# Performance work log

Hardware: AMD Instinct MI355X
Metric: run time of the kernel (lower is better)

Reference implementation:

```python
import jax, jax.numpy as jnp
import numpy as np

BSZ, T, D_IN, P, H, D_OUT = 8, 4096, 512, 256, 256, 512


def setup_inputs() -> dict:
    key = jax.random.key(0)
    ks = jax.random.split(key, 8)
    x_seq = jax.random.normal(ks[0], (BSZ, T, D_IN), dtype=jnp.float32)
    # stable diagonal transition: |a| < 1 so the 4096-step recurrence does not blow up
    a = jax.random.uniform(ks[1], (H,), minval=-0.99, maxval=0.99, dtype=jnp.float32)
    B = jax.random.normal(ks[2], (P, H), dtype=jnp.float32) * 0.05
    C = jax.random.normal(ks[3], (H, P), dtype=jnp.float32) * 0.05
    Wi = jax.random.normal(ks[4], (P, D_IN), dtype=jnp.float32) * 0.05
    bi = jax.random.normal(ks[5], (P,), dtype=jnp.float32) * 0.05
    Wo = jax.random.normal(ks[6], (D_OUT, P), dtype=jnp.float32) * 0.05
    bo = jax.random.normal(ks[7], (D_OUT,), dtype=jnp.float32) * 0.05
    return {"x_seq": x_seq, "a": a, "B": B, "C": C, "Wi": Wi, "bi": bi, "Wo": Wo, "bo": bo}


def reference(x_seq, a, B, C, Wi, bi, Wo, bo):
    # proj_in + relu (eqx.nn.Linear: y = W @ x + b), vmapped over batch and time
    x_proj = jax.nn.relu(jnp.einsum("btd,pd->btp", x_seq, Wi) + bi)  # [Bsz,T,P]
    # precompute driving input u_t = B^T x_t for every step
    u = jnp.einsum("btp,ph->bth", x_proj, B)  # [Bsz,T,H]
    u_t = jnp.swapaxes(u, 0, 1)  # [T,Bsz,H] (scan over time)

    def step(h, u_step):  # h: [Bsz,H]
        h = a * h + u_step
        return h, h

    h0 = jnp.zeros((x_seq.shape[0], a.shape[0]), dtype=x_seq.dtype)
    _, hs = jax.lax.scan(step, h0, u_t)  # hs: [T,Bsz,H]
    # y_t = C^T h_t, then proj_out
    y_seq = jnp.einsum("tbh,hp->btp", hs, C)  # [Bsz,T,P]
    y_out = jnp.einsum("btp,op->bto", y_seq, Wo) + bo  # [Bsz,T,D_out]
    return y_out
```

## Files before the change

### kernel.cpp

```cpp
#include <hip/hip_runtime.h>

#define BSZN 8
#define TT 4096
#define DIN 512
#define PP 256
#define HHH 256
#define DOUT 512
#define LCH 64
#define NCH (TT / LCH)
#define NBLK (BSZN * NCH)
#define XPS 264
#define AST 136

typedef __attribute__((ext_vector_type(8))) short bf16x8;
typedef __attribute__((ext_vector_type(4))) float f32x4;

#define GLOBAL_AS __attribute__((address_space(1)))
#define LDS_AS __attribute__((address_space(3)))

static __device__ __forceinline__ void gld_lds16(const void* g, void* l) {
  __builtin_amdgcn_global_load_lds((const GLOBAL_AS unsigned int*)g,
                                   (LDS_AS unsigned int*)l, 16, 0, 0);
}

static __device__ __forceinline__ unsigned short f2bf(float x) {
  union { float f; unsigned u; } t{x};
  unsigned r = t.u + 0x7fffu + ((t.u >> 16) & 1u);
  return (unsigned short)(r >> 16);
}

static __device__ __forceinline__ float ld_carry(const float* p) {
  return __hip_atomic_load(p, __ATOMIC_RELAXED, __HIP_MEMORY_SCOPE_AGENT);
}


__global__ __launch_bounds__(256) void prep_k(
    const float* __restrict__ Wi, const float* __restrict__ Wo,
    const float* __restrict__ Cm, const float* __restrict__ Bm,
    unsigned short* __restrict__ Wi_t, unsigned short* __restrict__ B_t,
    unsigned short* __restrict__ C_t, unsigned short* __restrict__ Wo_t,
    int* __restrict__ flag_g) {
  const int b = blockIdx.x, tid = threadIdx.x;
  if (b < 128) {
    const int idx = b * 1024 + tid * 4;
    const int row = idx >> 9, d = idx & 511;
    const float4 v = *(const float4*)(Wi + idx);
    uint2 w;
    w.x = (unsigned)f2bf(v.x) | ((unsigned)f2bf(v.y) << 16);
    w.y = (unsigned)f2bf(v.z) | ((unsigned)f2bf(v.w) << 16);
    const int tile = d >> 5, kc = (d >> 3) & 3, s = (kc + (row >> 1)) & 3;
    *(uint2*)(Wi_t + tile * 8192 + row * 32 + s * 8 + (d & 7)) = w;
  } else if (b < 192) {
    const int f = (b - 128) * 256 + tid;
    const int p = f >> 6, h = (f & 63) * 4;
    const float4 v = *(const float4*)(Bm + (size_t)p * HHH + h);
    const float vv[4] = {v.x, v.y, v.z, v.w};
    const int tile = p >> 5, kc = (p >> 3) & 3;
#pragma unroll
    for (int j = 0; j < 4; ++j) {
      const int row = h + j, s = (kc + (row >> 1)) & 3;
      B_t[tile * 8192 + row * 32 + s * 8 + (p & 7)] = f2bf(vv[j]);
    }
  } else if (b < 256) {
    const int f = (b - 192) * 256 + tid;
    const int h = f >> 6, p = (f & 63) * 4;
    const float4 v = *(const float4*)(Cm + (size_t)h * PP + p);
    const float vv[4] = {v.x, v.y, v.z, v.w};
    const int tile = h >> 5, kc = (h >> 3) & 3;
#pragma unroll
    for (int j = 0; j < 4; ++j) {
      const int row = p + j, s = (kc + (row >> 1)) & 3;
      C_t[tile * 8192 + row * 32 + s * 8 + (h & 7)] = f2bf(vv[j]);
    }
  } else if (b < 384) {
    const int idx = (b - 256) * 1024 + tid * 4;
    const int o = idx >> 8, p = idx & 255;
    const float4 v = *(const float4*)(Wo + idx);
    uint2 w;
    w.x = (unsigned)f2bf(v.x) | ((unsigned)f2bf(v.y) << 16);
    w.y = (unsigned)f2bf(v.z) | ((unsigned)f2bf(v.w) << 16);
    const int tile = p >> 5, kc = (p >> 3) & 3, s = (kc + (o >> 1)) & 3;
    *(uint2*)(Wo_t + tile * 16384 + o * 32 + s * 8 + (p & 7)) = w;
  } else {
    flag_g[tid] = 0;
    flag_g[tid + 256] = 0;
  }
}

__global__ __launch_bounds__(256, 2) void s4_mega(
    const float* __restrict__ x, const float* __restrict__ a,
    const unsigned short* __restrict__ Wi_t, const float* __restrict__ bi,
    const unsigned short* __restrict__ B_t,
    const unsigned short* __restrict__ C_t,
    const unsigned short* __restrict__ Wo_t, const float* __restrict__ bo,
    float* __restrict__ out, float* __restrict__ carry_g,
    int* __restrict__ flag_g) {
  __shared__ alignas(16) char smem[67584];
  char* As = smem;
  unsigned short* xp = (unsigned short*)smem;
  char* TB = smem + 33792;
  float* PL = (float*)(smem + 66560);

  const int tid = threadIdx.x, wave = tid >> 6, lane = tid & 63;
  const int l15 = lane & 15, q = lane >> 4;
  const int bc = blockIdx.x, b = bc >> 6, c = bc & (NCH - 1);
  const size_t row0 = (size_t)bc * LCH;
  const int wc = wave * 64;

  int wrot[4];
#pragma unroll
  for (int ni = 0; ni < 4; ++ni) {
    const int r = wc + ni * 16 + l15;
    wrot[ni] = r * 64 + (((q + (r >> 1)) & 3) << 4);
  }
  int crot[2][4];
#pragma unroll
  for (int g = 0; g < 2; ++g)
#pragma unroll
    for (int ni = 0; ni < 4; ++ni) {
      const int r = wave * 128 + g * 64 + ni * 16 + l15;
      crot[g][ni] = r * 64 + (((q + (r >> 1)) & 3) << 4);
    }
  int afb[4];
#pragma unroll
  for (int mi = 0; mi < 4; ++mi) afb[mi] = (mi * 16 + l15) * AST + q * 16;
  int xpb[4];
#pragma unroll
  for (int mi = 0; mi < 4; ++mi) xpb[mi] = (mi * 16 + l15) * XPS + q * 8;

  const int sbase = wave * 4096 + lane * 16;

  f32x4 acc[4][4];
#pragma unroll
  for (int i = 0; i < 4; ++i)
#pragma unroll
    for (int j = 0; j < 4; ++j) acc[i][j] = f32x4{0.f, 0.f, 0.f, 0.f};

  float4 xv[4];
#pragma unroll
  for (int i = 0; i < 4; ++i) {
    const int f = i * 256 + tid;
    xv[i] = *(const float4*)(x + (row0 + (f >> 4)) * DIN + (f & 15) * 4);
  }
  for (int t = 0; t < 8; ++t) {
#pragma unroll
    for (int i = 0; i < 4; ++i) {
      const int f = i * 256 + tid;
      uint2 w;
      w.x = (unsigned)f2bf(xv[i].x) | ((unsigned)f2bf(xv[i].y) << 16);
      w.y = (unsigned)f2bf(xv[i].z) | ((unsigned)f2bf(xv[i].w) << 16);
      *(uint2*)(As + (f >> 4) * AST + (f & 15) * 8) = w;
    }
    {
      const char* gw = (const char*)Wi_t + t * 32768 + sbase;
#pragma unroll
      for (int i = 0; i < 4; ++i) {
        gld_lds16(gw + i * 1024, TB + sbase + i * 1024);
        gld_lds16(gw + 16384 + i * 1024, TB + 16384 + sbase + i * 1024);
      }
    }
    __syncthreads();
    if (t < 7) {
#pragma unroll
      for (int i = 0; i < 4; ++i) {
        const int f = i * 256 + tid;
        xv[i] = *(const float4*)(x + (row0 + (f >> 4)) * DIN + (t + 1) * 64 +
                                 (f & 15) * 4);
      }
    }
    bf16x8 af[4][2], bfv[4][2];
#pragma unroll
    for (int mi = 0; mi < 4; ++mi) {
      af[mi][0] = *(const bf16x8*)(As + afb[mi]);
      af[mi][1] = *(const bf16x8*)(As + afb[mi] + 64);
    }
#pragma unroll
    for (int ni = 0; ni < 4; ++ni) {
      bfv[ni][0] = *(const bf16x8*)(TB + wrot[ni]);
      bfv[ni][1] = *(const bf16x8*)(TB + 16384 + wrot[ni]);
    }
#pragma unroll
    for (int kk = 0; kk < 2; ++kk)
#pragma unroll
      for (int mi = 0; mi < 4; ++mi)
#pragma unroll
        for (int ni = 0; ni < 4; ++ni)
          acc[mi][ni] = __builtin_amdgcn_mfma_f32_16x16x32_bf16(
              af[mi][kk], bfv[ni][kk], acc[mi][ni], 0, 0, 0);
    __syncthreads();
  }

  {
    const char* gw = (const char*)B_t + sbase;
#pragma unroll
    for (int i = 0; i < 4; ++i) {
      gld_lds16(gw + i * 1024, TB + sbase + i * 1024);
      gld_lds16(gw + 16384 + i * 1024, TB + 16384 + sbase + i * 1024);
    }
  }

#pragma unroll
  for (int ni = 0; ni < 4; ++ni) {
    const int col = wc + ni * 16 + l15;
    const float bb = bi[col];
#pragma unroll
    for (int mi = 0; mi < 4; ++mi)
#pragma unroll
      for (int reg = 0; reg < 4; ++reg) {
        const int row = mi * 16 + q * 4 + reg;
        xp[row * XPS + col] = f2bf(fmaxf(acc[mi][ni][reg] + bb, 0.f));
      }
  }

#pragma unroll
  for (int i = 0; i < 4; ++i)
#pragma unroll
    for (int j = 0; j < 4; ++j) acc[i][j] = f32x4{0.f, 0.f, 0.f, 0.f};
  for (int t = 0; t < 4; ++t) {
    if (t > 0) {
      const char* gw = (const char*)B_t + t * 32768 + sbase;
#pragma unroll
      for (int i = 0; i < 4; ++i) {
        gld_lds16(gw + i * 1024, TB + sbase + i * 1024);
        gld_lds16(gw + 16384 + i * 1024, TB + 16384 + sbase + i * 1024);
      }
    }
    __syncthreads();
    bf16x8 af[4][2], bfv[4][2];
#pragma unroll
    for (int mi = 0; mi < 4; ++mi) {
      af[mi][0] = *(const bf16x8*)(xp + xpb[mi] + t * 64);
      af[mi][1] = *(const bf16x8*)(xp + xpb[mi] + t * 64 + 32);
    }
#pragma unroll
    for (int ni = 0; ni < 4; ++ni) {
      bfv[ni][0] = *(const bf16x8*)(TB + wrot[ni]);
      bfv[ni][1] = *(const bf16x8*)(TB + 16384 + wrot[ni]);
    }
#pragma unroll
    for (int kk = 0; kk < 2; ++kk)
#pragma unroll
      for (int mi = 0; mi < 4; ++mi)
#pragma unroll
        for (int ni = 0; ni < 4; ++ni)
          acc[mi][ni] = __builtin_amdgcn_mfma_f32_16x16x32_bf16(
              af[mi][kk], bfv[ni][kk], acc[mi][ni], 0, 0, 0);
    __syncthreads();
  }

  float aC[4], Wz[4];
#pragma unroll
  for (int ni = 0; ni < 4; ++ni) aC[ni] = a[wc + ni * 16 + l15];
#pragma unroll
  for (int ni = 0; ni < 4; ++ni) {
    const float A = aC[ni];
    const float A2 = A * A, A4 = A2 * A2, A8 = A4 * A4, A16 = A8 * A8;
    const float A4q = ((q & 1) ? A4 : 1.f) * ((q & 2) ? A8 : 1.f);
    float W = 0.f;
#pragma unroll
    for (int mi = 0; mi < 4; ++mi) {
      f32x4 v = acc[mi][ni];
      v.y = fmaf(A, v.x, v.y);
      v.z = fmaf(A, v.y, v.z);
      v.w = fmaf(A, v.z, v.w);
      const float E = v.w;
      const float E0 = __shfl(E, l15, 64);
      const float E1 = __shfl(E, l15 + 16, 64);
      const float E2 = __shfl(E, l15 + 32, 64);
      const float E3 = __shfl(E, l15 + 48, 64);
      const float s1 = E0, s2 = fmaf(A4, s1, E1), s3 = fmaf(A4, s2, E2);
      const float s4 = fmaf(A4, s3, E3);
      const float Sq = (q == 0) ? 0.f : (q == 1) ? s1 : (q == 2) ? s2 : s3;
      const float sin_ = fmaf(A4q, W, Sq);
      v.x = fmaf(A, sin_, v.x);
      v.y = fmaf(A2, sin_, v.y);
      v.z = fmaf(A2 * A, sin_, v.z);
      v.w = fmaf(A4, sin_, v.w);
      acc[mi][ni] = v;
      W = fmaf(A16, W, s4);
    }
    Wz[ni] = W;
  }
  if (q == 0) {
#pragma unroll
    for (int ni = 0; ni < 4; ++ni)
      __hip_atomic_store(&carry_g[(size_t)bc * HHH + wc + ni * 16 + l15],
                         Wz[ni], __ATOMIC_RELAXED, __HIP_MEMORY_SCOPE_AGENT);
  }
  __syncthreads();
  if (tid == 0) {
    __threadfence();
    __hip_atomic_store(&flag_g[bc], 1, __ATOMIC_RELEASE,
                       __HIP_MEMORY_SCOPE_AGENT);
  }
  {
    const char* gw = (const char*)C_t + sbase;
#pragma unroll
    for (int i = 0; i < 4; ++i) {
      gld_lds16(gw + i * 1024, TB + sbase + i * 1024);
      gld_lds16(gw + 16384 + i * 1024, TB + 16384 + sbase + i * 1024);
    }
  }
  if (tid < c) {
    while (__hip_atomic_load(&flag_g[b * NCH + tid], __ATOMIC_ACQUIRE,
                             __HIP_MEMORY_SCOPE_AGENT) == 0)
      __builtin_amdgcn_s_sleep(32);
  }
  __syncthreads();
  {
    const int colp = tid;
    const float A = a[colp];
    float t1 = A;
#pragma unroll
    for (int j = 0; j < 6; ++j) t1 *= t1;
    const float A64 = t1, A128 = A64 * A64, A256 = A128 * A128;
    const float A512 = A256 * A256;
    const float* cg = carry_g + (size_t)b * NCH * HHH + colp;
    float P = 0.f;
    int j = 0;
    for (; j + 8 <= c; j += 8) {
      float cv[8];
#pragma unroll
      for (int i = 0; i < 8; ++i) cv[i] = ld_carry(cg + (size_t)(j + i) * HHH);
      float u = cv[0];
#pragma unroll
      for (int i = 1; i < 8; ++i) u = fmaf(A64, u, cv[i]);
      P = fmaf(A512, P, u);
    }
    for (; j < c; ++j) P = fmaf(A64, P, ld_carry(cg + (size_t)j * HHH));
    PL[colp] = P;
  }
  __syncthreads();
#pragma unroll
  for (int ni = 0; ni < 4; ++ni) {
    const float A = aC[ni];
    const float A2 = A * A, A4 = A2 * A2, A8 = A4 * A4, A16 = A8 * A8;
    const float A4q = ((q & 1) ? A4 : 1.f) * ((q & 2) ? A8 : 1.f);
    const float P = PL[wc + ni * 16 + l15];
    float fm = A4q * A * P;
#pragma unroll
    for (int mi = 0; mi < 4; ++mi) {
      f32x4 v = acc[mi][ni];
      v.x += fm;
      v.y = fmaf(A, fm, v.y);
      v.z = fmaf(A2, fm, v.z);
      v.w = fmaf(A2 * A, fm, v.w);
      acc[mi][ni] = v;
      fm *= A16;
    }
  }
  __syncthreads();

  unsigned short* hsL = (unsigned short*)smem;
#pragma unroll
  for (int ni = 0; ni < 4; ++ni) {
    const int col = wc + ni * 16 + l15;
#pragma unroll
    for (int mi = 0; mi < 4; ++mi)
#pragma unroll
      for (int reg = 0; reg < 4; ++reg)
        hsL[(mi * 16 + q * 4 + reg) * XPS + col] = f2bf(acc[mi][ni][reg]);
  }
#pragma unroll
  for (int i = 0; i < 4; ++i)
#pragma unroll
    for (int j = 0; j < 4; ++j) acc[i][j] = f32x4{0.f, 0.f, 0.f, 0.f};
  for (int t = 0; t < 4; ++t) {
    if (t > 0) {
      const char* gw = (const char*)C_t + t * 32768 + sbase;
#pragma unroll
      for (int i = 0; i < 4; ++i) {
        gld_lds16(gw + i * 1024, TB + sbase + i * 1024);
        gld_lds16(gw + 16384 + i * 1024, TB + 16384 + sbase + i * 1024);
      }
    }
    __syncthreads();
    bf16x8 af[4][2], bfv[4][2];
#pragma unroll
    for (int mi = 0; mi < 4; ++mi) {
      af[mi][0] = *(const bf16x8*)(hsL + xpb[mi] + t * 64);
      af[mi][1] = *(const bf16x8*)(hsL + xpb[mi] + t * 64 + 32);
    }
#pragma unroll
    for (int ni = 0; ni < 4; ++ni) {
      bfv[ni][0] = *(const bf16x8*)(TB + wrot[ni]);
      bfv[ni][1] = *(const bf16x8*)(TB + 16384 + wrot[ni]);
    }
#pragma unroll
    for (int kk = 0; kk < 2; ++kk)
#pragma unroll
      for (int mi = 0; mi < 4; ++mi)
#pragma unroll
        for (int ni = 0; ni < 4; ++ni)
          acc[mi][ni] = __builtin_amdgcn_mfma_f32_16x16x32_bf16(
              af[mi][kk], bfv[ni][kk], acc[mi][ni], 0, 0, 0);
    __syncthreads();
  }

  {
    const char* gw = (const char*)Wo_t + wave * 8192 + lane * 16;
#pragma unroll
    for (int i = 0; i < 8; ++i)
      gld_lds16(gw + i * 1024, TB + wave * 8192 + lane * 16 + i * 1024);
  }
#pragma unroll
  for (int ni = 0; ni < 4; ++ni) {
    const int col = wc + ni * 16 + l15;
#pragma unroll
    for (int mi = 0; mi < 4; ++mi)
#pragma unroll
      for (int reg = 0; reg < 4; ++reg)
        hsL[(mi * 16 + q * 4 + reg) * XPS + col] = f2bf(acc[mi][ni][reg]);
  }

  f32x4 oacc[2][4][4];
#pragma unroll
  for (int g = 0; g < 2; ++g)
#pragma unroll
    for (int i = 0; i < 4; ++i)
#pragma unroll
      for (int j = 0; j < 4; ++j) oacc[g][i][j] = f32x4{0.f, 0.f, 0.f, 0.f};
  for (int t = 0; t < 8; ++t) {
    if (t > 0) {
      const char* gw = (const char*)Wo_t + t * 32768 + wave * 8192 + lane * 16;
#pragma unroll
      for (int i = 0; i < 8; ++i)
        gld_lds16(gw + i * 1024, TB + wave * 8192 + lane * 16 + i * 1024);
    }
    __syncthreads();
    bf16x8 af[4], bfv[2][4];
#pragma unroll
    for (int mi = 0; mi < 4; ++mi)
      af[mi] = *(const bf16x8*)(hsL + xpb[mi] + t * 32);
#pragma unroll
    for (int g = 0; g < 2; ++g)
#pragma unroll
      for (int ni = 0; ni < 4; ++ni)
        bfv[g][ni] = *(const bf16x8*)(TB + crot[g][ni]);
#pragma unroll
    for (int g = 0; g < 2; ++g)
#pragma unroll
      for (int mi = 0; mi < 4; ++mi)
#pragma unroll
        for (int ni = 0; ni < 4; ++ni)
          oacc[g][mi][ni] = __builtin_amdgcn_mfma_f32_16x16x32_bf16(
              af[mi], bfv[g][ni], oacc[g][mi][ni], 0, 0, 0);
    __syncthreads();
  }
#pragma unroll
  for (int g = 0; g < 2; ++g)
#pragma unroll
    for (int ni = 0; ni < 4; ++ni) {
      const int ocol = wave * 128 + g * 64 + ni * 16 + l15;
      const float bb = bo[ocol];
#pragma unroll
      for (int mi = 0; mi < 4; ++mi)
#pragma unroll
        for (int reg = 0; reg < 4; ++reg) {
          const int row = mi * 16 + q * 4 + reg;
          out[(row0 + row) * DOUT + ocol] = oacc[g][mi][ni][reg] + bb;
        }
    }
}

extern "C" void kernel_launch(void* const* d_in, const int* in_sizes, int n_in,
                              void* d_out, int out_size, void* d_ws,
                              size_t ws_size, hipStream_t stream) {
  const float* x  = (const float*)d_in[0];
  const float* a  = (const float*)d_in[1];
  const float* Bm = (const float*)d_in[2];
  const float* Cm = (const float*)d_in[3];
  const float* Wi = (const float*)d_in[4];
  const float* bi = (const float*)d_in[5];
  const float* Wo = (const float*)d_in[6];
  const float* bo = (const float*)d_in[7];
  float* out = (float*)d_out;

  char* ws = (char*)d_ws;
  unsigned short* Wi_t = (unsigned short*)ws; ws += (size_t)PP * DIN * 2;
  unsigned short* B_t  = (unsigned short*)ws; ws += (size_t)HHH * PP * 2;
  unsigned short* C_t  = (unsigned short*)ws; ws += (size_t)HHH * PP * 2;
  unsigned short* Wo_t = (unsigned short*)ws; ws += (size_t)DOUT * PP * 2;
  float* carry_g = (float*)ws; ws += (size_t)NBLK * HHH * 4;
  int* flag_g = (int*)ws;

  prep_k<<<385, 256, 0, stream>>>(Wi, Wo, Cm, Bm, Wi_t, B_t, C_t, Wo_t,
                                  flag_g);
  s4_mega<<<NBLK, 256, 0, stream>>>(x, a, Wi_t, bi, B_t, C_t, Wo_t, bo, out,
                                    carry_g, flag_g);
}
```

Before: 189.7 us.

## Split fused scan kernel into scan, prefix, and output kernels

```diff
diff --git a/kernel.cpp b/kernel.cpp
--- a/kernel.cpp
+++ b/kernel.cpp
@@ -29,17 +29,12 @@
   return (unsigned short)(r >> 16);
 }
 
-static __device__ __forceinline__ float ld_carry(const float* p) {
-  return __hip_atomic_load(p, __ATOMIC_RELAXED, __HIP_MEMORY_SCOPE_AGENT);
-}
-
 
 __global__ __launch_bounds__(256) void prep_k(
     const float* __restrict__ Wi, const float* __restrict__ Wo,
     const float* __restrict__ Cm, const float* __restrict__ Bm,
     unsigned short* __restrict__ Wi_t, unsigned short* __restrict__ B_t,
-    unsigned short* __restrict__ C_t, unsigned short* __restrict__ Wo_t,
-    int* __restrict__ flag_g) {
+    unsigned short* __restrict__ C_t, unsigned short* __restrict__ Wo_t) {
   const int b = blockIdx.x, tid = threadIdx.x;
   if (b < 128) {
     const int idx = b * 1024 + tid * 4;
@@ -72,7 +67,7 @@
       const int row = p + j, s = (kc + (row >> 1)) & 3;
       C_t[tile * 8192 + row * 32 + s * 8 + (h & 7)] = f2bf(vv[j]);
     }
-  } else if (b < 384) {
+  } else {
     const int idx = (b - 256) * 1024 + tid * 4;
     const int o = idx >> 8, p = idx & 255;
     const float4 v = *(const float4*)(Wo + idx);
@@ -81,29 +76,22 @@
     w.y = (unsigned)f2bf(v.z) | ((unsigned)f2bf(v.w) << 16);
     const int tile = p >> 5, kc = (p >> 3) & 3, s = (kc + (o >> 1)) & 3;
     *(uint2*)(Wo_t + tile * 16384 + o * 32 + s * 8 + (p & 7)) = w;
-  } else {
-    flag_g[tid] = 0;
-    flag_g[tid + 256] = 0;
-  }
-}
-
-__global__ __launch_bounds__(256, 2) void s4_mega(
+  }
+}
+
+__global__ __launch_bounds__(256, 2) void s4_scan(
     const float* __restrict__ x, const float* __restrict__ a,
     const unsigned short* __restrict__ Wi_t, const float* __restrict__ bi,
-    const unsigned short* __restrict__ B_t,
-    const unsigned short* __restrict__ C_t,
-    const unsigned short* __restrict__ Wo_t, const float* __restrict__ bo,
-    float* __restrict__ out, float* __restrict__ carry_g,
-    int* __restrict__ flag_g) {
-  __shared__ alignas(16) char smem[67584];
+    const unsigned short* __restrict__ B_t, float* __restrict__ hs0_g,
+    float* __restrict__ carry_g) {
+  __shared__ alignas(16) char smem[66560];
   char* As = smem;
   unsigned short* xp = (unsigned short*)smem;
   char* TB = smem + 33792;
-  float* PL = (float*)(smem + 66560);
 
   const int tid = threadIdx.x, wave = tid >> 6, lane = tid & 63;
   const int l15 = lane & 15, q = lane >> 4;
-  const int bc = blockIdx.x, b = bc >> 6, c = bc & (NCH - 1);
+  const int bc = blockIdx.x;
   const size_t row0 = (size_t)bc * LCH;
   const int wc = wave * 64;
 
@@ -113,14 +101,6 @@
     const int r = wc + ni * 16 + l15;
     wrot[ni] = r * 64 + (((q + (r >> 1)) & 3) << 4);
   }
-  int crot[2][4];
-#pragma unroll
-  for (int g = 0; g < 2; ++g)
-#pragma unroll
-    for (int ni = 0; ni < 4; ++ni) {
-      const int r = wave * 128 + g * 64 + ni * 16 + l15;
-      crot[g][ni] = r * 64 + (((q + (r >> 1)) & 3) << 4);
-    }
   int afb[4];
 #pragma unroll
   for (int mi = 0; mi < 4; ++mi) afb[mi] = (mi * 16 + l15) * AST + q * 16;
@@ -284,15 +264,76 @@
   if (q == 0) {
 #pragma unroll
     for (int ni = 0; ni < 4; ++ni)
-      __hip_atomic_store(&carry_g[(size_t)bc * HHH + wc + ni * 16 + l15],
-                         Wz[ni], __ATOMIC_RELAXED, __HIP_MEMORY_SCOPE_AGENT);
-  }
-  __syncthreads();
-  if (tid == 0) {
-    __threadfence();
-    __hip_atomic_store(&flag_g[bc], 1, __ATOMIC_RELEASE,
-                       __HIP_MEMORY_SCOPE_AGENT);
-  }
+      carry_g[(size_t)bc * HHH + wc + ni * 16 + l15] = Wz[ni];
+  }
+#pragma unroll
+  for (int ni = 0; ni < 4; ++ni) {
+    const int col = wc + ni * 16 + l15;
+#pragma unroll
+    for (int mi = 0; mi < 4; ++mi)
+#pragma unroll
+      for (int reg = 0; reg < 4; ++reg) {
+        const int row = mi * 16 + q * 4 + reg;
+        hs0_g[(row0 + row) * HHH + col] = acc[mi][ni][reg];
+      }
+  }
+}
+
+__global__ __launch_bounds__(256) void s4_prefix(
+    const float* __restrict__ a, const float* __restrict__ carry_g,
+    float* __restrict__ P_g) {
+  const int b = blockIdx.x, t = threadIdx.x;
+  float A = a[t];
+#pragma unroll
+  for (int j = 0; j < 6; ++j) A *= A;
+  const float* cg = carry_g + (size_t)b * NCH * HHH + t;
+  float* pg = P_g + (size_t)b * NCH * HHH + t;
+  float cv[NCH];
+#pragma unroll
+  for (int c = 0; c < NCH; ++c) cv[c] = cg[(size_t)c * HHH];
+  float P = 0.f;
+#pragma unroll
+  for (int c = 0; c < NCH; ++c) {
+    pg[(size_t)c * HHH] = P;
+    P = fmaf(A, P, cv[c]);
+  }
+}
+
+__global__ __launch_bounds__(256, 2) void s4_out(
+    const float* __restrict__ a, const float* __restrict__ hs0_g,
+    const float* __restrict__ P_g, const unsigned short* __restrict__ C_t,
+    const unsigned short* __restrict__ Wo_t, const float* __restrict__ bo,
+    float* __restrict__ out) {
+  __shared__ alignas(16) char smem[66560];
+  unsigned short* hsL = (unsigned short*)smem;
+  char* TB = smem + 33792;
+
+  const int tid = threadIdx.x, wave = tid >> 6, lane = tid & 63;
+  const int l15 = lane & 15, q = lane >> 4;
+  const int bc = blockIdx.x;
+  const size_t row0 = (size_t)bc * LCH;
+  const int wc = wave * 64;
+
+  int wrot[4];
+#pragma unroll
+  for (int ni = 0; ni < 4; ++ni) {
+    const int r = wc + ni * 16 + l15;
+    wrot[ni] = r * 64 + (((q + (r >> 1)) & 3) << 4);
+  }
+  int crot[2][4];
+#pragma unroll
+  for (int g = 0; g < 2; ++g)
+#pragma unroll
+    for (int ni = 0; ni < 4; ++ni) {
+      const int r = wave * 128 + g * 64 + ni * 16 + l15;
+      crot[g][ni] = r * 64 + (((q + (r >> 1)) & 3) << 4);
+    }
+  int xpb[4];
+#pragma unroll
+  for (int mi = 0; mi < 4; ++mi) xpb[mi] = (mi * 16 + l15) * XPS + q * 8;
+
+  const int sbase = wave * 4096 + lane * 16;
+
   {
     const char* gw = (const char*)C_t + sbase;
 #pragma unroll
@@ -301,42 +342,24 @@
       gld_lds16(gw + 16384 + i * 1024, TB + 16384 + sbase + i * 1024);
     }
   }
-  if (tid < c) {
-    while (__hip_atomic_load(&flag_g[b * NCH + tid], __ATOMIC_ACQUIRE,
-                             __HIP_MEMORY_SCOPE_AGENT) == 0)
-      __builtin_amdgcn_s_sleep(32);
-  }
-  __syncthreads();
-  {
-    const int colp = tid;
-    const float A = a[colp];
-    float t1 = A;
-#pragma unroll
-    for (int j = 0; j < 6; ++j) t1 *= t1;
-    const float A64 = t1, A128 = A64 * A64, A256 = A128 * A128;
-    const float A512 = A256 * A256;
-    const float* cg = carry_g + (size_t)b * NCH * HHH + colp;
-    float P = 0.f;
-    int j = 0;
-    for (; j + 8 <= c; j += 8) {
-      float cv[8];
-#pragma unroll
-      for (int i = 0; i < 8; ++i) cv[i] = ld_carry(cg + (size_t)(j + i) * HHH);
-      float u = cv[0];
-#pragma unroll
-      for (int i = 1; i < 8; ++i) u = fmaf(A64, u, cv[i]);
-      P = fmaf(A512, P, u);
-    }
-    for (; j < c; ++j) P = fmaf(A64, P, ld_carry(cg + (size_t)j * HHH));
-    PL[colp] = P;
-  }
-  __syncthreads();
-#pragma unroll
-  for (int ni = 0; ni < 4; ++ni) {
-    const float A = aC[ni];
+
+  f32x4 acc[4][4];
+#pragma unroll
+  for (int ni = 0; ni < 4; ++ni) {
+    const int col = wc + ni * 16 + l15;
+#pragma unroll
+    for (int mi = 0; mi < 4; ++mi)
+#pragma unroll
+      for (int reg = 0; reg < 4; ++reg)
+        acc[mi][ni][reg] = hs0_g[(row0 + mi * 16 + q * 4 + reg) * HHH + col];
+  }
+#pragma unroll
+  for (int ni = 0; ni < 4; ++ni) {
+    const int col = wc + ni * 16 + l15;
+    const float A = a[col];
+    const float P = P_g[(size_t)bc * HHH + col];
     const float A2 = A * A, A4 = A2 * A2, A8 = A4 * A4, A16 = A8 * A8;
     const float A4q = ((q & 1) ? A4 : 1.f) * ((q & 2) ? A8 : 1.f);
-    const float P = PL[wc + ni * 16 + l15];
     float fm = A4q * A * P;
 #pragma unroll
     for (int mi = 0; mi < 4; ++mi) {
@@ -349,9 +372,6 @@
       fm *= A16;
     }
   }
-  __syncthreads();
-
-  unsigned short* hsL = (unsigned short*)smem;
 #pragma unroll
   for (int ni = 0; ni < 4; ++ni) {
     const int col = wc + ni * 16 + l15;
@@ -361,6 +381,7 @@
       for (int reg = 0; reg < 4; ++reg)
         hsL[(mi * 16 + q * 4 + reg) * XPS + col] = f2bf(acc[mi][ni][reg]);
   }
+
 #pragma unroll
   for (int i = 0; i < 4; ++i)
 #pragma unroll
@@ -482,10 +503,11 @@
   unsigned short* C_t  = (unsigned short*)ws; ws += (size_t)HHH * PP * 2;
   unsigned short* Wo_t = (unsigned short*)ws; ws += (size_t)DOUT * PP * 2;
   float* carry_g = (float*)ws; ws += (size_t)NBLK * HHH * 4;
-  int* flag_g = (int*)ws;
-
-  prep_k<<<385, 256, 0, stream>>>(Wi, Wo, Cm, Bm, Wi_t, B_t, C_t, Wo_t,
-                                  flag_g);
-  s4_mega<<<NBLK, 256, 0, stream>>>(x, a, Wi_t, bi, B_t, C_t, Wo_t, bo, out,
-                                    carry_g, flag_g);
-}
+  float* P_g     = (float*)ws; ws += (size_t)NBLK * HHH * 4;
+  float* hs0_g   = (float*)ws;
+
+  prep_k<<<384, 256, 0, stream>>>(Wi, Wo, Cm, Bm, Wi_t, B_t, C_t, Wo_t);
+  s4_scan<<<NBLK, 256, 0, stream>>>(x, a, Wi_t, bi, B_t, hs0_g, carry_g);
+  s4_prefix<<<BSZN, 256, 0, stream>>>(a, carry_g, P_g);
+  s4_out<<<NBLK, 256, 0, stream>>>(a, hs0_g, P_g, C_t, Wo_t, bo, out);
+}
```

After: 172.5 us. 9.0% less time.
